# Kernel optimization log

Hardware: AMD Instinct MI355X
Metric: run time of the kernel (lower is better)

## Reference

```python
import jax, jax.numpy as jnp
import numpy as np

NUM_QUERIES = 10000
NUM_CLASSES = 2048
IOU_THRESH = 0.5


def setup_inputs() -> dict:
    key = jax.random.key(0)
    k1, k2, k3, k4 = jax.random.split(key, 4)
    return {
        "pred_logits": jax.random.normal(k1, (1, NUM_QUERIES, NUM_CLASSES), dtype=jnp.float32),
        "pred_boxes": jax.random.uniform(k2, (1, NUM_QUERIES, 4), dtype=jnp.float32),
        "cls_logits": jax.random.normal(k3, (1, NUM_CLASSES), dtype=jnp.float32),
        "target_sizes": jax.random.randint(k4, (1, 2), 480, 1333, dtype=jnp.int64),
    }


def box_cxcywh_to_xyxy(b):
    cx, cy, w, h = b[..., 0], b[..., 1], b[..., 2], b[..., 3]
    return jnp.stack([cx - 0.5 * w, cy - 0.5 * h, cx + 0.5 * w, cy + 0.5 * h], axis=-1)


def nms_keep(boxes, scores, iou_thresh):
    """Greedy NMS; returns a boolean keep mask over the N boxes (xyxy)."""
    n = boxes.shape[0]
    order = jnp.argsort(-scores)
    bs = boxes[order]  # [N,4] sorted by score desc
    areas = jnp.clip(bs[:, 2] - bs[:, 0], 0.0) * jnp.clip(bs[:, 3] - bs[:, 1], 0.0)
    idx = jnp.arange(n)

    def body(i, state):
        keep_s, active = state
        alive = active[i]
        keep_s = keep_s.at[i].set(alive)
        # IoU of box i against all boxes
        lt = jnp.maximum(bs[i, :2], bs[:, :2])
        rb = jnp.minimum(bs[i, 2:], bs[:, 2:])
        wh = jnp.clip(rb - lt, 0.0)
        inter = wh[:, 0] * wh[:, 1]
        iou = inter / (areas[i] + areas - inter)
        suppress = (iou > iou_thresh) & (idx > i) & alive
        return keep_s, active & (~suppress)

    keep_s, _ = jax.lax.fori_loop(
        0, n, body, (jnp.zeros(n, dtype=bool), jnp.ones(n, dtype=bool))
    )
    # map back from sorted order to original order
    return jnp.zeros(n, dtype=bool).at[order].set(keep_s)


def reference(pred_logits, pred_boxes, cls_logits, target_sizes):
    # class scores / labels
    prob = jax.nn.softmax(pred_logits, axis=-1)          # [B,Q,C]
    scores = prob.max(axis=-1)                           # [B,Q]
    labels = prob.argmax(axis=-1)                        # [B,Q]
    cls_preds = jnp.argmax(cls_logits, axis=1)           # [B]

    # boxes: cxcywh -> xyxy, clamp to [0,1], scale to image size
    boxes = jnp.clip(box_cxcywh_to_xyxy(pred_boxes), 0.0, 1.0)  # [B,Q,4]
    ts = target_sizes.astype(jnp.float32)
    img_h, img_w = ts[:, 0], ts[:, 1]
    scale_fct = jnp.stack([img_w, img_h, img_w, img_h], axis=1)  # [B,4]
    boxes = boxes * scale_fct[:, None, :]

    # greedy NMS on batch 0 (module only supports this path for B=1)
    keep = nms_keep(boxes[0], scores.reshape(-1), IOU_THRESH)    # [Q] bool

    return scores[0], labels[0], boxes[0], keep, cls_preds
```

## Files before the change

kernel.cpp:

```cpp
#include <hip/hip_runtime.h>
#include <stdint.h>

#define NQ 10000
#define NC 2048
#define NW 157
#define IOU_TH 0.5f


__global__ __launch_bounds__(256) void k_scores(const float* __restrict__ logits,
        float* __restrict__ out_scores, float* __restrict__ out_labels,
        float* __restrict__ ws_scores) {
    int wave = threadIdx.x >> 6;
    int lane = threadIdx.x & 63;
    int q = blockIdx.x * 4 + wave;
    if (q >= NQ) return;
    const float* row = logits + (size_t)q * NC;
    float4 v[8];
    float m = -3.4e38f;
    int am = 0;
    #pragma unroll
    for (int k = 0; k < 8; k++) {
        int idx = k * 256 + lane * 4;
        v[k] = *(const float4*)(row + idx);
        if (v[k].x > m) { m = v[k].x; am = idx; }
        if (v[k].y > m) { m = v[k].y; am = idx + 1; }
        if (v[k].z > m) { m = v[k].z; am = idx + 2; }
        if (v[k].w > m) { m = v[k].w; am = idx + 3; }
    }
    #pragma unroll
    for (int off = 32; off >= 1; off >>= 1) {
        float om = __shfl_xor(m, off);
        int   oa = __shfl_xor(am, off);
        if (om > m || (om == m && oa < am)) { m = om; am = oa; }
    }
    float s = 0.f;
    #pragma unroll
    for (int k = 0; k < 8; k++) {
        s += expf(v[k].x - m);
        s += expf(v[k].y - m);
        s += expf(v[k].z - m);
        s += expf(v[k].w - m);
    }
    #pragma unroll
    for (int off = 32; off >= 1; off >>= 1) s += __shfl_xor(s, off);
    if (lane == 0) {
        float sc = 1.0f / s;
        out_scores[q] = sc;
        out_labels[q] = (float)am;
        ws_scores[q]  = sc;
    }
}

__global__ __launch_bounds__(256) void k_cls(const float* __restrict__ cls,
                                             float* __restrict__ out) {
    float m = -3.4e38f; int am = 0x7fffffff;
    for (int idx = threadIdx.x; idx < NC; idx += 256) {
        float x = cls[idx];
        if (x > m) { m = x; am = idx; }
    }
    int lane = threadIdx.x & 63, wave = threadIdx.x >> 6;
    #pragma unroll
    for (int off = 32; off >= 1; off >>= 1) {
        float om = __shfl_xor(m, off); int oa = __shfl_xor(am, off);
        if (om > m || (om == m && oa < am)) { m = om; am = oa; }
    }
    __shared__ float sm[4]; __shared__ int sa[4];
    if (lane == 0) { sm[wave] = m; sa[wave] = am; }
    __syncthreads();
    if (threadIdx.x == 0) {
        for (int w = 1; w < 4; w++)
            if (sm[w] > m || (sm[w] == m && sa[w] < am)) { m = sm[w]; am = sa[w]; }
        out[0] = (float)am;
    }
}

__global__ __launch_bounds__(256) void k_boxes(const float* __restrict__ pb,
        const int* __restrict__ ts, float* __restrict__ out_boxes,
        float* __restrict__ boxes4, int* __restrict__ rank) {
    #pragma clang fp contract(off)
    int i = blockIdx.x * 256 + threadIdx.x;
    if (i >= NQ) return;
    rank[i] = 0;
    int a0 = ts[0], a1 = ts[1];
    int ih, iw;
    if (a1 == 0) { ih = a0; iw = ts[2]; } else { ih = a0; iw = a1; }
    float sh = (float)ih, sw = (float)iw;
    float4 b = *(const float4*)(pb + i * 4);
    float x1 = b.x - 0.5f * b.z;
    float y1 = b.y - 0.5f * b.w;
    float x2 = b.x + 0.5f * b.z;
    float y2 = b.y + 0.5f * b.w;
    x1 = fminf(fmaxf(x1, 0.f), 1.f) * sw;
    y1 = fminf(fmaxf(y1, 0.f), 1.f) * sh;
    x2 = fminf(fmaxf(x2, 0.f), 1.f) * sw;
    y2 = fminf(fmaxf(y2, 0.f), 1.f) * sh;
    float4 o = make_float4(x1, y1, x2, y2);
    *(float4*)(out_boxes + i * 4) = o;
    *(float4*)(boxes4 + i * 4) = o;
}

__global__ __launch_bounds__(256) void k_count(const float* __restrict__ scores,
                                               int* __restrict__ rank) {
    __shared__ float sc[2000];
    int jbase = blockIdx.y * 2000;
    int jn = min(2000, NQ - jbase);
    for (int t = threadIdx.x; t < jn; t += 256) sc[t] = scores[jbase + t];
    __syncthreads();
    int i = blockIdx.x * 256 + threadIdx.x;
    if (i >= NQ) return;
    float si = scores[i];
    int cnt = 0;
    for (int jj = 0; jj < jn; jj++) {
        float sj = sc[jj];
        int j = jbase + jj;
        cnt += (sj > si) || (sj == si && j < i);
    }
    if (cnt) atomicAdd(&rank[i], cnt);
}

__global__ __launch_bounds__(256) void k_scatter(const float* __restrict__ boxes4,
        const int* __restrict__ rank, int* __restrict__ order,
        float* __restrict__ sx1, float* __restrict__ sy1,
        float* __restrict__ sx2, float* __restrict__ sy2,
        float* __restrict__ sarea) {
    #pragma clang fp contract(off)
    int i = blockIdx.x * 256 + threadIdx.x;
    if (i >= NQ) return;
    int r = rank[i];
    order[r] = i;
    float4 b = *(const float4*)(boxes4 + i * 4);
    sx1[r] = b.x; sy1[r] = b.y; sx2[r] = b.z; sy2[r] = b.w;
    sarea[r] = fmaxf(b.z - b.x, 0.f) * fmaxf(b.w - b.y, 0.f);
}

__global__ __launch_bounds__(64) void k_mask(const float* __restrict__ sx1,
        const float* __restrict__ sy1, const float* __restrict__ sx2,
        const float* __restrict__ sy2, const float* __restrict__ sarea,
        unsigned long long* __restrict__ mask) {
    #pragma clang fp contract(off)
    int rb = blockIdx.x, cb = blockIdx.y;
    if (cb < rb) return;
    int t = threadIdx.x;
    __shared__ float cx1[64], cy1[64], cx2[64], cy2[64], ca[64];
    int j0 = cb * 64 + t;
    if (j0 < NQ) { cx1[t]=sx1[j0]; cy1[t]=sy1[j0]; cx2[t]=sx2[j0]; cy2[t]=sy2[j0]; ca[t]=sarea[j0]; }
    __syncthreads();
    int i = rb * 64 + t;
    if (i >= NQ) return;
    float xi1 = sx1[i], yi1 = sy1[i], xi2 = sx2[i], yi2 = sy2[i], ai = sarea[i];
    int ncol = min(64, NQ - cb * 64);
    unsigned long long word = 0;
    for (int jj = 0; jj < ncol; jj++) {
        int j = cb * 64 + jj;
        float lx = fmaxf(xi1, cx1[jj]);
        float ly = fmaxf(yi1, cy1[jj]);
        float rx = fminf(xi2, cx2[jj]);
        float ry = fminf(yi2, cy2[jj]);
        float w = fmaxf(rx - lx, 0.f);
        float h = fmaxf(ry - ly, 0.f);
        float inter = w * h;
        float denom = (ai + ca[jj]) - inter;
        float iou = inter / denom;
        bool sup = (iou > IOU_TH) && (j > i);
        word |= ((unsigned long long)(sup ? 1u : 0u)) << jj;
    }
    mask[(size_t)i * NW + cb] = word;
}

__global__ __launch_bounds__(256, 1) void k_scan(const unsigned long long* __restrict__ mask,
        const int* __restrict__ order, float* __restrict__ out_keep) {
    __shared__ unsigned long long rem[NW];
    __shared__ unsigned long long keepw[NW];
    __shared__ unsigned long long dgbuf[2][64];
    __shared__ unsigned long long ccbuf[2][64];
    __shared__ unsigned long long sh_kept;

    const int tid  = threadIdx.x;
    const int wave = tid >> 6;
    const int lane = tid & 63;

    for (int w = tid; w < NW; w += 256) rem[w] = 0;

    if (wave == 0) {
        const unsigned long long* rp = mask + (size_t)lane * NW;
        dgbuf[0][lane] = rp[0];
        ccbuf[0][lane] = rp[1];
    }
    __syncthreads();

    uint64_t p0=0,p1=0,p2=0,p3=0,p4=0,p5=0,p6=0,p7=0;
    uint64_t p8=0,p9=0,p10=0,p11=0,p12=0,p13=0,p14=0,p15=0;
    uint64_t pextra = 0;
    int pw = -1;

    for (int c = 0; c < NW; c++) {
        uint64_t dn = 0, ccn = 0;
        if (wave == 0) {
            if (c + 1 < NW) {
                int i2 = (c + 1) * 64 + lane;
                if (i2 < NQ) {
                    const unsigned long long* rp = mask + (size_t)i2 * NW;
                    dn = rp[c + 1];
                    if (c + 2 < NW) ccn = rp[c + 2];
                }
            }
            uint64_t t64 = rem[c];
            uint32_t clo = (uint32_t)__builtin_amdgcn_readfirstlane((int)(uint32_t)t64);
            uint32_t chi = (uint32_t)__builtin_amdgcn_readfirstlane((int)(uint32_t)(t64 >> 32));
            uint64_t cur = ((uint64_t)chi << 32) | clo;
            int nvalid = min(64, NQ - c * 64);
            if (nvalid < 64) cur |= (~0ull) << nvalid;

            uint64_t dgv = dgbuf[c & 1][lane];
            uint32_t dvlo = (uint32_t)dgv, dvhi = (uint32_t)(dgv >> 32);

            uint64_t alive = ~cur;
            uint64_t kept  = 0;
            while (alive) {
                int b = (int)__builtin_ctzll(alive);
                uint32_t dlo = (uint32_t)__builtin_amdgcn_readlane((int)dvlo, b);
                uint32_t dhi = (uint32_t)__builtin_amdgcn_readlane((int)dvhi, b);
                uint64_t d = ((uint64_t)dhi << 32) | dlo;
                kept  |= 1ull << b;
                cur   |= d;
                alive &= ~(d | (1ull << b));
            }
            if (tid == 0) { sh_kept = kept; keepw[c] = cur; }
        } else {
            if (pw >= 0) {
                uint64_t pacc = ((p0|p1)|(p2|p3)) | ((p4|p5)|(p6|p7));
                pacc |= ((p8|p9)|(p10|p11)) | ((p12|p13)|(p14|p15));
                pacc |= pextra;
                if (pacc) atomicOr(&rem[pw], (unsigned long long)pacc);
            }
            pw = -1;
        }
        __syncthreads();

        uint64_t kts;
        {
            uint64_t t64 = sh_kept;
            uint32_t klo = (uint32_t)__builtin_amdgcn_readfirstlane((int)(uint32_t)t64);
            uint32_t khi = (uint32_t)__builtin_amdgcn_readfirstlane((int)(uint32_t)(t64 >> 32));
            kts = ((uint64_t)khi << 32) | klo;
        }

        if (wave == 0) {
            if (c + 1 < NW) {
                uint64_t ccv = ccbuf[c & 1][lane];
                if ((kts >> lane) & 1ull) atomicOr(&rem[c + 1], (unsigned long long)ccv);
                dgbuf[(c + 1) & 1][lane] = dn;
                if (c + 2 < NW) ccbuf[(c + 1) & 1][lane] = ccn;
            }
        } else {
            int w = c + 2 + (tid - 64);
            if (kts && w < NW) {
                const unsigned long long* base = mask + (size_t)(c * 64) * NW + w;
                uint64_t km = kts;
                int r_first = (int)__builtin_ctzll(km);
                int r;
                r = km ? (int)__builtin_ctzll(km) : r_first; if (km) km &= km - 1; p0  = base[(size_t)r * NW];
                r = km ? (int)__builtin_ctzll(km) : r_first; if (km) km &= km - 1; p1  = base[(size_t)r * NW];
                r = km ? (int)__builtin_ctzll(km) : r_first; if (km) km &= km - 1; p2  = base[(size_t)r * NW];
                r = km ? (int)__builtin_ctzll(km) : r_first; if (km) km &= km - 1; p3  = base[(size_t)r * NW];
                r = km ? (int)__builtin_ctzll(km) : r_first; if (km) km &= km - 1; p4  = base[(size_t)r * NW];
                r = km ? (int)__builtin_ctzll(km) : r_first; if (km) km &= km - 1; p5  = base[(size_t)r * NW];
                r = km ? (int)__builtin_ctzll(km) : r_first; if (km) km &= km - 1; p6  = base[(size_t)r * NW];
                r = km ? (int)__builtin_ctzll(km) : r_first; if (km) km &= km - 1; p7  = base[(size_t)r * NW];
                r = km ? (int)__builtin_ctzll(km) : r_first; if (km) km &= km - 1; p8  = base[(size_t)r * NW];
                r = km ? (int)__builtin_ctzll(km) : r_first; if (km) km &= km - 1; p9  = base[(size_t)r * NW];
                r = km ? (int)__builtin_ctzll(km) : r_first; if (km) km &= km - 1; p10 = base[(size_t)r * NW];
                r = km ? (int)__builtin_ctzll(km) : r_first; if (km) km &= km - 1; p11 = base[(size_t)r * NW];
                r = km ? (int)__builtin_ctzll(km) : r_first; if (km) km &= km - 1; p12 = base[(size_t)r * NW];
                r = km ? (int)__builtin_ctzll(km) : r_first; if (km) km &= km - 1; p13 = base[(size_t)r * NW];
                r = km ? (int)__builtin_ctzll(km) : r_first; if (km) km &= km - 1; p14 = base[(size_t)r * NW];
                r = km ? (int)__builtin_ctzll(km) : r_first; if (km) km &= km - 1; p15 = base[(size_t)r * NW];
                pextra = 0;
                while (km) {
                    uint64_t x0=0,x1=0,x2=0,x3=0,x4=0,x5=0,x6=0,x7=0;
                    if (km) { r=(int)__builtin_ctzll(km); km&=km-1; x0=base[(size_t)r*NW]; }
                    if (km) { r=(int)__builtin_ctzll(km); km&=km-1; x1=base[(size_t)r*NW]; }
                    if (km) { r=(int)__builtin_ctzll(km); km&=km-1; x2=base[(size_t)r*NW]; }
                    if (km) { r=(int)__builtin_ctzll(km); km&=km-1; x3=base[(size_t)r*NW]; }
                    if (km) { r=(int)__builtin_ctzll(km); km&=km-1; x4=base[(size_t)r*NW]; }
                    if (km) { r=(int)__builtin_ctzll(km); km&=km-1; x5=base[(size_t)r*NW]; }
                    if (km) { r=(int)__builtin_ctzll(km); km&=km-1; x6=base[(size_t)r*NW]; }
                    if (km) { r=(int)__builtin_ctzll(km); km&=km-1; x7=base[(size_t)r*NW]; }
                    pextra |= (x0|x1)|(x2|x3)|((x4|x5)|(x6|x7));
                }
                pw = w;
            } else {
                pw = -1; pextra = 0;
            }
        }
        __syncthreads();
    }

    for (int si = tid; si < NQ; si += 256) {
        unsigned long long kw = keepw[si >> 6];
        out_keep[order[si]] = ((kw >> (si & 63)) & 1ull) ? 0.f : 1.f;
    }
}

extern "C" void kernel_launch(void* const* d_in, const int* in_sizes, int n_in,
                              void* d_out, int out_size, void* d_ws, size_t ws_size,
                              hipStream_t stream) {
    const float* pred_logits = (const float*)d_in[0];
    const float* pred_boxes  = (const float*)d_in[1];
    const float* cls_logits  = (const float*)d_in[2];
    const int*   tsizes      = (const int*)d_in[3];

    float* out = (float*)d_out;
    float* out_scores = out;
    float* out_labels = out + 10000;
    float* out_boxes  = out + 20000;
    float* out_keep   = out + 60000;
    float* out_cls    = out + 70000;

    char* ws = (char*)d_ws;
    float* ws_scores = (float*)(ws + 0);
    int*   rank      = (int*)  (ws + 40000);
    float* boxes4    = (float*)(ws + 80000);
    float* sx1       = (float*)(ws + 240000);
    float* sy1       = (float*)(ws + 280000);
    float* sx2       = (float*)(ws + 320000);
    float* sy2       = (float*)(ws + 360000);
    float* sarea     = (float*)(ws + 400000);
    int*   order     = (int*)  (ws + 440000);
    unsigned long long* mask = (unsigned long long*)(ws + 480000);

    k_scores<<<2500, 256, 0, stream>>>(pred_logits, out_scores, out_labels, ws_scores);
    k_cls<<<1, 256, 0, stream>>>(cls_logits, out_cls);
    k_boxes<<<40, 256, 0, stream>>>(pred_boxes, tsizes, out_boxes, boxes4, rank);
    k_count<<<dim3(40, 5), 256, 0, stream>>>(ws_scores, rank);
    k_scatter<<<40, 256, 0, stream>>>(boxes4, rank, order, sx1, sy1, sx2, sy2, sarea);
    k_mask<<<dim3(157, 157), 64, 0, stream>>>(sx1, sy1, sx2, sy2, sarea, mask);
    k_scan<<<1, 256, 0, stream>>>(mask, order, out_keep);
}
```

Baseline: 429.9 us.

## Fuse front kernels, triangular mask grid, vectorize rank count, batch NMS scan

```diff
diff --git a/kernel.cpp b/kernel.cpp
--- a/kernel.cpp
+++ b/kernel.cpp
@@ -1,119 +1,129 @@
 #include <hip/hip_runtime.h>
 #include <stdint.h>
+#include <math.h>
 
 #define NQ 10000
 #define NC 2048
 #define NW 157
+#define NTRI 12403
 #define IOU_TH 0.5f
 
 
-__global__ __launch_bounds__(256) void k_scores(const float* __restrict__ logits,
+__global__ __launch_bounds__(256) void k_front(const float* __restrict__ logits,
+        const float* __restrict__ cls, const float* __restrict__ pb,
+        const int* __restrict__ ts,
         float* __restrict__ out_scores, float* __restrict__ out_labels,
-        float* __restrict__ ws_scores) {
-    int wave = threadIdx.x >> 6;
-    int lane = threadIdx.x & 63;
-    int q = blockIdx.x * 4 + wave;
-    if (q >= NQ) return;
-    const float* row = logits + (size_t)q * NC;
-    float4 v[8];
-    float m = -3.4e38f;
-    int am = 0;
-    #pragma unroll
-    for (int k = 0; k < 8; k++) {
-        int idx = k * 256 + lane * 4;
-        v[k] = *(const float4*)(row + idx);
-        if (v[k].x > m) { m = v[k].x; am = idx; }
-        if (v[k].y > m) { m = v[k].y; am = idx + 1; }
-        if (v[k].z > m) { m = v[k].z; am = idx + 2; }
-        if (v[k].w > m) { m = v[k].w; am = idx + 3; }
-    }
-    #pragma unroll
-    for (int off = 32; off >= 1; off >>= 1) {
-        float om = __shfl_xor(m, off);
-        int   oa = __shfl_xor(am, off);
-        if (om > m || (om == m && oa < am)) { m = om; am = oa; }
-    }
-    float s = 0.f;
-    #pragma unroll
-    for (int k = 0; k < 8; k++) {
-        s += expf(v[k].x - m);
-        s += expf(v[k].y - m);
-        s += expf(v[k].z - m);
-        s += expf(v[k].w - m);
-    }
-    #pragma unroll
-    for (int off = 32; off >= 1; off >>= 1) s += __shfl_xor(s, off);
-    if (lane == 0) {
-        float sc = 1.0f / s;
-        out_scores[q] = sc;
-        out_labels[q] = (float)am;
-        ws_scores[q]  = sc;
-    }
-}
-
-__global__ __launch_bounds__(256) void k_cls(const float* __restrict__ cls,
-                                             float* __restrict__ out) {
-    float m = -3.4e38f; int am = 0x7fffffff;
-    for (int idx = threadIdx.x; idx < NC; idx += 256) {
-        float x = cls[idx];
-        if (x > m) { m = x; am = idx; }
-    }
-    int lane = threadIdx.x & 63, wave = threadIdx.x >> 6;
-    #pragma unroll
-    for (int off = 32; off >= 1; off >>= 1) {
-        float om = __shfl_xor(m, off); int oa = __shfl_xor(am, off);
-        if (om > m || (om == m && oa < am)) { m = om; am = oa; }
-    }
-    __shared__ float sm[4]; __shared__ int sa[4];
-    if (lane == 0) { sm[wave] = m; sa[wave] = am; }
-    __syncthreads();
-    if (threadIdx.x == 0) {
-        for (int w = 1; w < 4; w++)
-            if (sm[w] > m || (sm[w] == m && sa[w] < am)) { m = sm[w]; am = sa[w]; }
-        out[0] = (float)am;
-    }
-}
-
-__global__ __launch_bounds__(256) void k_boxes(const float* __restrict__ pb,
-        const int* __restrict__ ts, float* __restrict__ out_boxes,
-        float* __restrict__ boxes4, int* __restrict__ rank) {
-    #pragma clang fp contract(off)
-    int i = blockIdx.x * 256 + threadIdx.x;
-    if (i >= NQ) return;
-    rank[i] = 0;
-    int a0 = ts[0], a1 = ts[1];
-    int ih, iw;
-    if (a1 == 0) { ih = a0; iw = ts[2]; } else { ih = a0; iw = a1; }
-    float sh = (float)ih, sw = (float)iw;
-    float4 b = *(const float4*)(pb + i * 4);
-    float x1 = b.x - 0.5f * b.z;
-    float y1 = b.y - 0.5f * b.w;
-    float x2 = b.x + 0.5f * b.z;
-    float y2 = b.y + 0.5f * b.w;
-    x1 = fminf(fmaxf(x1, 0.f), 1.f) * sw;
-    y1 = fminf(fmaxf(y1, 0.f), 1.f) * sh;
-    x2 = fminf(fmaxf(x2, 0.f), 1.f) * sw;
-    y2 = fminf(fmaxf(y2, 0.f), 1.f) * sh;
-    float4 o = make_float4(x1, y1, x2, y2);
-    *(float4*)(out_boxes + i * 4) = o;
-    *(float4*)(boxes4 + i * 4) = o;
+        float* __restrict__ out_cls, float* __restrict__ out_boxes,
+        float* __restrict__ ws_scores, float* __restrict__ boxes4,
+        int* __restrict__ rank) {
+    int bx = blockIdx.x;
+    if (bx < 2500) {
+        int wave = threadIdx.x >> 6;
+        int lane = threadIdx.x & 63;
+        int q = bx * 4 + wave;
+        if (q >= NQ) return;
+        const float* row = logits + (size_t)q * NC;
+        float4 v[8];
+        float m = -3.4e38f;
+        int am = 0;
+        #pragma unroll
+        for (int k = 0; k < 8; k++) {
+            int idx = k * 256 + lane * 4;
+            v[k] = *(const float4*)(row + idx);
+            if (v[k].x > m) { m = v[k].x; am = idx; }
+            if (v[k].y > m) { m = v[k].y; am = idx + 1; }
+            if (v[k].z > m) { m = v[k].z; am = idx + 2; }
+            if (v[k].w > m) { m = v[k].w; am = idx + 3; }
+        }
+        #pragma unroll
+        for (int off = 32; off >= 1; off >>= 1) {
+            float om = __shfl_xor(m, off);
+            int   oa = __shfl_xor(am, off);
+            if (om > m || (om == m && oa < am)) { m = om; am = oa; }
+        }
+        float s = 0.f;
+        #pragma unroll
+        for (int k = 0; k < 8; k++) {
+            s += expf(v[k].x - m);
+            s += expf(v[k].y - m);
+            s += expf(v[k].z - m);
+            s += expf(v[k].w - m);
+        }
+        #pragma unroll
+        for (int off = 32; off >= 1; off >>= 1) s += __shfl_xor(s, off);
+        if (lane == 0) {
+            float sc = 1.0f / s;
+            out_scores[q] = sc;
+            out_labels[q] = (float)am;
+            ws_scores[q]  = sc;
+        }
+        return;
+    }
+    if (bx == 2500) {
+        float m = -3.4e38f; int am = 0x7fffffff;
+        for (int idx = threadIdx.x; idx < NC; idx += 256) {
+            float x = cls[idx];
+            if (x > m) { m = x; am = idx; }
+        }
+        int lane = threadIdx.x & 63, wave = threadIdx.x >> 6;
+        #pragma unroll
+        for (int off = 32; off >= 1; off >>= 1) {
+            float om = __shfl_xor(m, off); int oa = __shfl_xor(am, off);
+            if (om > m || (om == m && oa < am)) { m = om; am = oa; }
+        }
+        __shared__ float sm[4]; __shared__ int sa[4];
+        if (lane == 0) { sm[wave] = m; sa[wave] = am; }
+        __syncthreads();
+        if (threadIdx.x == 0) {
+            for (int w = 1; w < 4; w++)
+                if (sm[w] > m || (sm[w] == m && sa[w] < am)) { m = sm[w]; am = sa[w]; }
+            out_cls[0] = (float)am;
+        }
+        return;
+    }
+    {
+        #pragma clang fp contract(off)
+        int i = (bx - 2501) * 256 + threadIdx.x;
+        if (i >= NQ) return;
+        rank[i] = 0;
+        int a0 = ts[0], a1 = ts[1];
+        int ih, iw;
+        if (a1 == 0) { ih = a0; iw = ts[2]; } else { ih = a0; iw = a1; }
+        float sh = (float)ih, sw = (float)iw;
+        float4 b = *(const float4*)(pb + i * 4);
+        float x1 = b.x - 0.5f * b.z;
+        float y1 = b.y - 0.5f * b.w;
+        float x2 = b.x + 0.5f * b.z;
+        float y2 = b.y + 0.5f * b.w;
+        x1 = fminf(fmaxf(x1, 0.f), 1.f) * sw;
+        y1 = fminf(fmaxf(y1, 0.f), 1.f) * sh;
+        x2 = fminf(fmaxf(x2, 0.f), 1.f) * sw;
+        y2 = fminf(fmaxf(y2, 0.f), 1.f) * sh;
+        float4 o = make_float4(x1, y1, x2, y2);
+        *(float4*)(out_boxes + i * 4) = o;
+        *(float4*)(boxes4 + i * 4) = o;
+    }
 }
 
 __global__ __launch_bounds__(256) void k_count(const float* __restrict__ scores,
                                                int* __restrict__ rank) {
-    __shared__ float sc[2000];
+    __shared__ float4 sc4[500];
     int jbase = blockIdx.y * 2000;
-    int jn = min(2000, NQ - jbase);
-    for (int t = threadIdx.x; t < jn; t += 256) sc[t] = scores[jbase + t];
+    const float4* src = (const float4*)(scores + jbase);
+    for (int t = threadIdx.x; t < 500; t += 256) sc4[t] = src[t];
     __syncthreads();
     int i = blockIdx.x * 256 + threadIdx.x;
     if (i >= NQ) return;
     float si = scores[i];
     int cnt = 0;
-    for (int jj = 0; jj < jn; jj++) {
-        float sj = sc[jj];
-        int j = jbase + jj;
-        cnt += (sj > si) || (sj == si && j < i);
+    #pragma unroll 2
+    for (int q = 0; q < 500; q++) {
+        float4 v = sc4[q];
+        int j = jbase + 4 * q;
+        cnt += (v.x > si) || (v.x == si && j     < i);
+        cnt += (v.y > si) || (v.y == si && j + 1 < i);
+        cnt += (v.z > si) || (v.z == si && j + 2 < i);
+        cnt += (v.w > si) || (v.w == si && j + 3 < i);
     }
     if (cnt) atomicAdd(&rank[i], cnt);
 }
@@ -138,8 +148,13 @@
         const float* __restrict__ sy2, const float* __restrict__ sarea,
         unsigned long long* __restrict__ mask) {
     #pragma clang fp contract(off)
-    int rb = blockIdx.x, cb = blockIdx.y;
-    if (cb < rb) return;
+    int tri = blockIdx.x;
+    int rb = (int)((2.0 * NW + 1.0
+              - sqrt((double)((2 * NW + 1) * (2 * NW + 1) - 8 * tri))) * 0.5);
+    while (rb > 0 && rb * NW - rb * (rb - 1) / 2 > tri) rb--;
+    while ((rb + 1) * NW - (rb + 1) * rb / 2 <= tri) rb++;
+    int cb = rb + (tri - (rb * NW - rb * (rb - 1) / 2));
+
     int t = threadIdx.x;
     __shared__ float cx1[64], cy1[64], cx2[64], cy2[64], ca[64];
     int j0 = cb * 64 + t;
@@ -167,6 +182,17 @@
     mask[(size_t)i * NW + cb] = word;
 }
 
+__device__ __forceinline__ unsigned long long bcast64(unsigned long long v) {
+    uint32_t lo = (uint32_t)__builtin_amdgcn_readfirstlane((int)(uint32_t)v);
+    uint32_t hi = (uint32_t)__builtin_amdgcn_readfirstlane((int)(uint32_t)(v >> 32));
+    return ((unsigned long long)hi << 32) | lo;
+}
+
+__device__ __forceinline__ uint64_t rl64(uint32_t lo, uint32_t hi, int b) {
+    return ((uint64_t)(uint32_t)__builtin_amdgcn_readlane((int)hi, b) << 32)
+         | (uint32_t)__builtin_amdgcn_readlane((int)lo, b);
+}
+
 __global__ __launch_bounds__(256, 1) void k_scan(const unsigned long long* __restrict__ mask,
         const int* __restrict__ order, float* __restrict__ out_keep) {
     __shared__ unsigned long long rem[NW];
@@ -204,10 +230,7 @@
                     if (c + 2 < NW) ccn = rp[c + 2];
                 }
             }
-            uint64_t t64 = rem[c];
-            uint32_t clo = (uint32_t)__builtin_amdgcn_readfirstlane((int)(uint32_t)t64);
-            uint32_t chi = (uint32_t)__builtin_amdgcn_readfirstlane((int)(uint32_t)(t64 >> 32));
-            uint64_t cur = ((uint64_t)chi << 32) | clo;
+            uint64_t cur = bcast64(rem[c]);
             int nvalid = min(64, NQ - c * 64);
             if (nvalid < 64) cur |= (~0ull) << nvalid;
 
@@ -217,13 +240,22 @@
             uint64_t alive = ~cur;
             uint64_t kept  = 0;
             while (alive) {
-                int b = (int)__builtin_ctzll(alive);
-                uint32_t dlo = (uint32_t)__builtin_amdgcn_readlane((int)dvlo, b);
-                uint32_t dhi = (uint32_t)__builtin_amdgcn_readlane((int)dvhi, b);
-                uint64_t d = ((uint64_t)dhi << 32) | dlo;
-                kept  |= 1ull << b;
-                cur   |= d;
-                alive &= ~(d | (1ull << b));
+                uint64_t t0 = alive;
+                int b0 = (int)__builtin_ctzll(t0); t0 &= t0 - 1;
+                int b1 = t0 ? (int)__builtin_ctzll(t0) : b0; t0 &= t0 - 1;
+                int b2 = t0 ? (int)__builtin_ctzll(t0) : b0; t0 &= t0 - 1;
+                int b3 = t0 ? (int)__builtin_ctzll(t0) : b0;
+                uint64_t d0 = rl64(dvlo, dvhi, b0);
+                uint64_t d1 = rl64(dvlo, dvhi, b1);
+                uint64_t d2 = rl64(dvlo, dvhi, b2);
+                uint64_t d3 = rl64(dvlo, dvhi, b3);
+                uint64_t sup = d0;
+                kept |= 1ull << b0;
+                if (!((sup >> b1) & 1ull)) { kept |= 1ull << b1; sup |= d1; }
+                if (!((sup >> b2) & 1ull)) { kept |= 1ull << b2; sup |= d2; }
+                if (!((sup >> b3) & 1ull)) { kept |= 1ull << b3; sup |= d3; }
+                cur   |= sup;
+                alive &= ~(sup | (1ull << b0) | (1ull << b1) | (1ull << b2) | (1ull << b3));
             }
             if (tid == 0) { sh_kept = kept; keepw[c] = cur; }
         } else {
@@ -240,15 +272,16 @@
         uint64_t kts;
         {
             uint64_t t64 = sh_kept;
-            uint32_t klo = (uint32_t)__builtin_amdgcn_readfirstlane((int)(uint32_t)t64);
-            uint32_t khi = (uint32_t)__builtin_amdgcn_readfirstlane((int)(uint32_t)(t64 >> 32));
-            kts = ((uint64_t)khi << 32) | klo;
+            kts = bcast64(t64);
         }
 
         if (wave == 0) {
             if (c + 1 < NW) {
                 uint64_t ccv = ccbuf[c & 1][lane];
-                if ((kts >> lane) & 1ull) atomicOr(&rem[c + 1], (unsigned long long)ccv);
+                uint64_t m = ((kts >> lane) & 1ull) ? ccv : 0;
+                #pragma unroll
+                for (int off = 32; off >= 1; off >>= 1) m |= __shfl_xor(m, off);
+                if (lane == 0) rem[c + 1] |= m;
                 dgbuf[(c + 1) & 1][lane] = dn;
                 if (c + 2 < NW) ccbuf[(c + 1) & 1][lane] = ccn;
             }
@@ -329,11 +362,11 @@
     int*   order     = (int*)  (ws + 440000);
     unsigned long long* mask = (unsigned long long*)(ws + 480000);
 
-    k_scores<<<2500, 256, 0, stream>>>(pred_logits, out_scores, out_labels, ws_scores);
-    k_cls<<<1, 256, 0, stream>>>(cls_logits, out_cls);
-    k_boxes<<<40, 256, 0, stream>>>(pred_boxes, tsizes, out_boxes, boxes4, rank);
+    k_front<<<2541, 256, 0, stream>>>(pred_logits, cls_logits, pred_boxes, tsizes,
+                                      out_scores, out_labels, out_cls, out_boxes,
+                                      ws_scores, boxes4, rank);
     k_count<<<dim3(40, 5), 256, 0, stream>>>(ws_scores, rank);
     k_scatter<<<40, 256, 0, stream>>>(boxes4, rank, order, sx1, sy1, sx2, sy2, sarea);
-    k_mask<<<dim3(157, 157), 64, 0, stream>>>(sx1, sy1, sx2, sy2, sarea, mask);
+    k_mask<<<NTRI, 64, 0, stream>>>(sx1, sy1, sx2, sy2, sarea, mask);
     k_scan<<<1, 256, 0, stream>>>(mask, order, out_keep);
 }
```

Result: faster. 418.9 us (-2.6%).
